# Kernel tuning notes

Hardware: AMD Instinct MI355X
Metric: run time of the kernel (lower is better)

The kernel has to match this reference:

```python
import jax, jax.numpy as jnp
import numpy as np

NUM_HEADS = 16
KEY_DIM = 64
NUM_FEATURES = 256
D_MODEL = NUM_HEADS * KEY_DIM
EPS = 1e-6


def softmax_kernel(data, proj):
    # data: [..., N, D], proj: [D, F]
    # Faithful to source: ratio uses proj.shape[0] (=D), matching the TF code.
    data_normalizer = 1.0 / jnp.sqrt(jnp.sqrt(jnp.asarray(data.shape[-1], data.dtype)))
    ratio = 1.0 / jnp.sqrt(jnp.asarray(proj.shape[0], data.dtype))
    data = data_normalizer * data
    data_dash = jnp.einsum('...nd,df->...nf', data, proj)
    diag = jnp.sum(jnp.square(data), axis=-1, keepdims=True)  # [..., N, 1]
    return ratio * (jnp.exp(data_dash - diag / 2.0) + EPS)


def setup_inputs() -> dict:
    key = jax.random.key(0)
    ks = jax.random.split(key, 12)
    B, N = 4, 4096
    s = 1.0 / np.sqrt(D_MODEL)
    inp = {
        'queries': jax.random.normal(ks[0], (B, N, D_MODEL), jnp.float32),
        'keys': jax.random.normal(ks[1], (B, N, D_MODEL), jnp.float32),
        'Wq': jax.random.normal(ks[2], (D_MODEL, D_MODEL), jnp.float32) * s,
        'bq': jnp.zeros((D_MODEL,), jnp.float32),
        'Wk': jax.random.normal(ks[3], (D_MODEL, D_MODEL), jnp.float32) * s,
        'bk': jnp.zeros((D_MODEL,), jnp.float32),
        'Wv': jax.random.normal(ks[4], (D_MODEL, D_MODEL), jnp.float32) * s,
        'bv': jnp.zeros((D_MODEL,), jnp.float32),
        'Wo': jax.random.normal(ks[5], (D_MODEL, D_MODEL), jnp.float32) * s,
        'bo': jnp.zeros((D_MODEL,), jnp.float32),
        # GlorotNormal for [KEY_DIM, NUM_FEATURES]
        'proj': jax.random.normal(ks[6], (KEY_DIM, NUM_FEATURES), jnp.float32)
                * np.sqrt(2.0 / (KEY_DIM + NUM_FEATURES)),
    }
    return inp


def reference(queries, keys, Wq, bq, Wk, bk, Wv, bv, Wo, bo, proj):
    # Original code uses x = queries for q, k, v (self-attention); keys arg unused.
    x = queries
    B, N, _ = x.shape
    H, D = NUM_HEADS, KEY_DIM

    def split_heads(t):
        return t.reshape(B, N, H, D).transpose(0, 2, 1, 3)  # [B,H,N,D]

    q = split_heads(x @ Wq + bq)
    k = split_heads(x @ Wk + bk)
    v = split_heads(x @ Wv + bv)

    q_prime = softmax_kernel(q, proj)  # [B,H,N,F]
    k_prime = softmax_kernel(k, proj)  # [B,H,N,F]

    kv = jnp.einsum('bhnf,bhnd->bhfd', k_prime, v)        # [B,H,F,D]
    qkv = jnp.einsum('bhnf,bhfd->bhnd', q_prime, kv)       # [B,H,N,D]
    k_sum = jnp.sum(k_prime, axis=2)                        # [B,H,F]
    norm = jnp.einsum('bhnf,bhf->bhn', q_prime, k_sum) + EPS
    qkv = qkv / norm[..., None]

    out = qkv.transpose(0, 2, 1, 3).reshape(B, N, H * D)    # [B,N,d_model]
    return out @ Wo + bo
```

## Files before the change

kernel.cpp:

```cpp
#include <hip/hip_runtime.h>

typedef __attribute__((ext_vector_type(8))) short short8;
typedef __attribute__((ext_vector_type(4))) float f32x4;

#define MFMA16 __builtin_amdgcn_mfma_f32_16x16x32_bf16

#define GLOAD16(gp, lp) __builtin_amdgcn_global_load_lds(                      \
    (const __attribute__((address_space(1))) void*)(gp),                       \
    (__attribute__((address_space(3))) void*)(lp), 16, 0, 0)

__device__ __forceinline__ unsigned short f2bf(float f) {
  unsigned int u = __float_as_uint(f);
  unsigned int r = u + 0x7fffu + ((u >> 16) & 1u);
  return (unsigned short)(r >> 16);
}
__device__ __forceinline__ float bf2f(unsigned short h) {
  return __uint_as_float(((unsigned int)h) << 16);
}

__global__ __launch_bounds__(256) void cast_x_kernel(
    const float* __restrict__ in, unsigned short* __restrict__ out, int n4) {
  int i = blockIdx.x * 256 + threadIdx.x;
  if (i >= n4) return;
  float4 v = reinterpret_cast<const float4*>(in)[i];
  ushort4 o;
  o.x = f2bf(v.x); o.y = f2bf(v.y); o.z = f2bf(v.z); o.w = f2bf(v.w);
  reinterpret_cast<ushort4*>(out)[i] = o;
}

__global__ __launch_bounds__(256) void tcast_f32_kernel(
    const float* __restrict__ in, unsigned short* __restrict__ out, int R, int C) {
  __shared__ float t[64][65];
  int c0 = blockIdx.x * 64, r0 = blockIdx.y * 64;
  int tx = threadIdx.x, ty = threadIdx.y;
#pragma unroll
  for (int i = 0; i < 16; ++i)
    t[ty + 4 * i][tx] = in[(size_t)(r0 + ty + 4 * i) * C + c0 + tx];
  __syncthreads();
#pragma unroll
  for (int i = 0; i < 16; ++i)
    out[(size_t)(c0 + ty + 4 * i) * R + r0 + tx] = f2bf(t[tx][ty + 4 * i]);
}

__global__ __launch_bounds__(256) void tcast4_kernel(
    const float* __restrict__ i0, const float* __restrict__ i1,
    const float* __restrict__ i2, const float* __restrict__ i3,
    unsigned short* __restrict__ o0, unsigned short* __restrict__ o1,
    unsigned short* __restrict__ o2, unsigned short* __restrict__ o3) {
  const float* in = i0; unsigned short* out = o0;
  if (blockIdx.z == 1) { in = i1; out = o1; }
  else if (blockIdx.z == 2) { in = i2; out = o2; }
  else if (blockIdx.z == 3) { in = i3; out = o3; }
  __shared__ float t[64][65];
  int c0 = blockIdx.x * 64, r0 = blockIdx.y * 64;
  int tx = threadIdx.x, ty = threadIdx.y;
#pragma unroll
  for (int i = 0; i < 16; ++i)
    t[ty + 4 * i][tx] = in[(size_t)(r0 + ty + 4 * i) * 1024 + c0 + tx];
  __syncthreads();
#pragma unroll
  for (int i = 0; i < 16; ++i)
    out[(size_t)(c0 + ty + 4 * i) * 1024 + r0 + tx] = f2bf(t[tx][ty + 4 * i]);
}

template <int OUTF>
__global__ __launch_bounds__(256) void gemm_bt_kernel(
    const unsigned short* __restrict__ A,
    const unsigned short* W0, const unsigned short* W1, const unsigned short* W2,
    const float* b0, const float* b1, const float* b2,
    void* o0, void* o1, void* o2) {
  constexpr int KD = 1024, ND = 1024;
  const unsigned short* W = W0; const float* bias = b0; void* op = o0;
  if (blockIdx.z == 1) { W = W1; bias = b1; op = o1; }
  else if (blockIdx.z == 2) { W = W2; bias = b2; op = o2; }

  __shared__ unsigned short lsA[128 * 32];
  __shared__ unsigned short lsB[128 * 32];
  extern __shared__ unsigned short tt[];
  int tid = threadIdx.x;
  int w = tid >> 6, lane = tid & 63;
  int m0 = blockIdx.x * 128, n0 = blockIdx.y * 128;
  int wm = (w >> 1) * 64, wn = (w & 1) * 64;

  int srow0 = (w * 2 + 0) * 16 + (lane >> 2);
  int srow1 = (w * 2 + 1) * 16 + (lane >> 2);
  int scol = (lane & 3) * 8;
  const unsigned short* gA0 = A + (size_t)(m0 + srow0) * KD + scol;
  const unsigned short* gA1 = A + (size_t)(m0 + srow1) * KD + scol;
  const unsigned short* gB0 = W + (size_t)(n0 + srow0) * KD + scol;
  const unsigned short* gB1 = W + (size_t)(n0 + srow1) * KD + scol;
  unsigned short* lA0 = &lsA[(w * 2 + 0) * 512];
  unsigned short* lA1 = &lsA[(w * 2 + 1) * 512];
  unsigned short* lB0 = &lsB[(w * 2 + 0) * 512];
  unsigned short* lB1 = &lsB[(w * 2 + 1) * 512];

  f32x4 acc[4][4];
#pragma unroll
  for (int fm = 0; fm < 4; ++fm)
#pragma unroll
    for (int fn = 0; fn < 4; ++fn) acc[fm][fn] = (f32x4){0.f, 0.f, 0.f, 0.f};

  for (int kt = 0; kt < KD; kt += 32) {
    GLOAD16(gA0 + kt, lA0);
    GLOAD16(gA1 + kt, lA1);
    GLOAD16(gB0 + kt, lB0);
    GLOAD16(gB1 + kt, lB1);
    __syncthreads();
    short8 af[4], bfr[4];
#pragma unroll
    for (int fm = 0; fm < 4; ++fm)
      af[fm] = *reinterpret_cast<const short8*>(
          &lsA[(wm + fm * 16 + (lane & 15)) * 32 + (lane >> 4) * 8]);
#pragma unroll
    for (int fn = 0; fn < 4; ++fn)
      bfr[fn] = *reinterpret_cast<const short8*>(
          &lsB[(wn + fn * 16 + (lane & 15)) * 32 + (lane >> 4) * 8]);
#pragma unroll
    for (int fm = 0; fm < 4; ++fm)
#pragma unroll
      for (int fn = 0; fn < 4; ++fn)
        acc[fm][fn] = MFMA16(af[fm], bfr[fn], acc[fm][fn], 0, 0, 0);
    __syncthreads();
  }

#pragma unroll
  for (int fn = 0; fn < 4; ++fn) {
    int coll = wn + fn * 16 + (lane & 15);
    float bv = bias[n0 + coll];
#pragma unroll
    for (int fm = 0; fm < 4; ++fm) {
#pragma unroll
      for (int j = 0; j < 4; ++j) {
        int rowl = wm + fm * 16 + (lane >> 4) * 4 + j;
        float v = acc[fm][fn][j] + bv;
        if constexpr (OUTF == 2) {
          tt[coll * 136 + rowl] = f2bf(v);
        } else if constexpr (OUTF == 1) {
          reinterpret_cast<float*>(op)[(size_t)(m0 + rowl) * ND + n0 + coll] = v;
        } else {
          reinterpret_cast<unsigned short*>(op)[(size_t)(m0 + rowl) * ND + n0 + coll] =
              f2bf(v);
        }
      }
    }
  }
  if constexpr (OUTF == 2) {
    __syncthreads();
    int b = m0 >> 12, tok0 = m0 & 4095;
    int c = tid >> 1, half = (tid & 1) * 64;
    unsigned short* dst = reinterpret_cast<unsigned short*>(op) +
                          (size_t)(b * 1024 + n0 + c) * 4096 + tok0 + half;
#pragma unroll
    for (int i = 0; i < 8; ++i) {
      short8 vv = *reinterpret_cast<const short8*>(&tt[c * 136 + half + i * 8]);
      *reinterpret_cast<short8*>(dst + i * 8) = vv;
    }
  }
}

__global__ __launch_bounds__(256) void kv_fused_kernel(
    const unsigned short* __restrict__ K, const unsigned short* __restrict__ PT,
    const unsigned short* __restrict__ VT,
    float* __restrict__ kvp0, float* __restrict__ kvp1, float* __restrict__ ksp) {
  __shared__ unsigned short kp[256 * 40];
  int s = blockIdx.x, bh = blockIdx.y, b = bh >> 4, h = bh & 15;
  int tid = threadIdx.x, w = tid >> 6, lane = tid & 63;
  int lo = lane & 15, hi = lane >> 4;
  int f0w = w * 64;
  float* kvp = (s < 8) ? kvp0 : kvp1;
  int sl = s & 7;

  short8 pb[4][2];
#pragma unroll
  for (int fn = 0; fn < 4; ++fn) {
    int f = f0w + fn * 16 + lo;
    pb[fn][0] = *reinterpret_cast<const short8*>(PT + (size_t)f * 64 + hi * 8);
    pb[fn][1] = *reinterpret_cast<const short8*>(PT + (size_t)f * 64 + 32 + hi * 8);
  }
  const unsigned short* vbase[4];
#pragma unroll
  for (int fn = 0; fn < 4; ++fn)
    vbase[fn] = VT + (size_t)(bh * 64 + fn * 16 + lo) * 4096;

  f32x4 acck[4][4];
#pragma unroll
  for (int fm = 0; fm < 4; ++fm)
#pragma unroll
    for (int fn = 0; fn < 4; ++fn) acck[fm][fn] = (f32x4){0.f, 0.f, 0.f, 0.f};
  float ks[4] = {0.f, 0.f, 0.f, 0.f};

  for (int c = 0; c < 8; ++c) {
    int n0 = s * 256 + c * 32;
    const unsigned short* Ab = K + (size_t)(b * 4096 + n0) * 1024 + h * 64;
    short8 af[2][2];
    float dp[2] = {0.f, 0.f};
#pragma unroll
    for (int fm = 0; fm < 2; ++fm)
#pragma unroll
      for (int kt = 0; kt < 2; ++kt) {
        af[fm][kt] = *reinterpret_cast<const short8*>(
            Ab + (size_t)(fm * 16 + lo) * 1024 + kt * 32 + hi * 8);
#pragma unroll
        for (int j = 0; j < 8; ++j) {
          float qv = bf2f((unsigned short)af[fm][kt][j]);
          dp[fm] += qv * qv;
        }
      }
#pragma unroll
    for (int fm = 0; fm < 2; ++fm) {
      dp[fm] += __shfl_xor(dp[fm], 16);
      dp[fm] += __shfl_xor(dp[fm], 32);
    }
    f32x4 accf[2][4];
#pragma unroll
    for (int fm = 0; fm < 2; ++fm)
#pragma unroll
      for (int fn = 0; fn < 4; ++fn) accf[fm][fn] = (f32x4){0.f, 0.f, 0.f, 0.f};
#pragma unroll
    for (int fn = 0; fn < 4; ++fn) {
      accf[0][fn] = MFMA16(af[0][0], pb[fn][0], accf[0][fn], 0, 0, 0);
      accf[0][fn] = MFMA16(af[0][1], pb[fn][1], accf[0][fn], 0, 0, 0);
      accf[1][fn] = MFMA16(af[1][0], pb[fn][0], accf[1][fn], 0, 0, 0);
      accf[1][fn] = MFMA16(af[1][1], pb[fn][1], accf[1][fn], 0, 0, 0);
    }
#pragma unroll
    for (int fm = 0; fm < 2; ++fm)
#pragma unroll
      for (int fn = 0; fn < 4; ++fn)
#pragma unroll
        for (int j = 0; j < 4; ++j) {
          float dg = __shfl(dp[fm], hi * 4 + j);
          float v = 0.125f *
                    (__expf(0.35355339059327373f * accf[fm][fn][j] - 0.0625f * dg) + 1e-6f);
          ks[fn] += v;
          kp[(f0w + fn * 16 + lo) * 40 + fm * 16 + hi * 4 + j] = f2bf(v);
        }
    short8 a2[4], b2[4];
#pragma unroll
    for (int fm = 0; fm < 4; ++fm)
      a2[fm] = *reinterpret_cast<const short8*>(&kp[(f0w + fm * 16 + lo) * 40 + hi * 8]);
#pragma unroll
    for (int fn = 0; fn < 4; ++fn)
      b2[fn] = *reinterpret_cast<const short8*>(vbase[fn] + n0 + hi * 8);
#pragma unroll
    for (int fm = 0; fm < 4; ++fm)
#pragma unroll
      for (int fn = 0; fn < 4; ++fn)
        acck[fm][fn] = MFMA16(a2[fm], b2[fn], acck[fm][fn], 0, 0, 0);
  }
#pragma unroll
  for (int fn = 0; fn < 4; ++fn) {
    float v = ks[fn];
    v += __shfl_xor(v, 16);
    v += __shfl_xor(v, 32);
    if (hi == 0)
      ksp[(size_t)(s * 64 + bh) * 256 + f0w + fn * 16 + lo] = v;
  }
#pragma unroll
  for (int fm = 0; fm < 4; ++fm)
#pragma unroll
    for (int fn = 0; fn < 4; ++fn)
#pragma unroll
      for (int j = 0; j < 4; ++j)
        kvp[((size_t)(sl * 64 + bh) * 256 + f0w + fm * 16 + hi * 4 + j) * 64 + fn * 16 + lo] =
            acck[fm][fn][j];
}

__global__ __launch_bounds__(256) void kvred_kernel(
    const float* __restrict__ kvp0, const float* __restrict__ kvp1,
    const float* __restrict__ ksp,
    unsigned short* __restrict__ kvT, float* __restrict__ ksum) {
  __shared__ float t[64][65];
  int bh = blockIdx.x, g = blockIdx.y, tid = threadIdx.x;
  int fbase = g * 64;
  int fo = tid >> 2, dq = (tid & 3) * 16;
  float sum[16];
#pragma unroll
  for (int i = 0; i < 16; ++i) sum[i] = 0.f;
#pragma unroll
  for (int s = 0; s < 16; ++s) {
    const float* base = ((s < 8) ? kvp0 : kvp1) +
                        ((size_t)((s & 7) * 64 + bh) * 256 + fbase + fo) * 64 + dq;
#pragma unroll
    for (int i = 0; i < 16; ++i) sum[i] += base[i];
  }
#pragma unroll
  for (int i = 0; i < 16; ++i) t[fo][dq + i] = sum[i];
  __syncthreads();
  int d = tid >> 2, fq = (tid & 3) * 16;
  unsigned short wv[16];
#pragma unroll
  for (int i = 0; i < 16; ++i) wv[i] = f2bf(t[fq + i][d]);
  unsigned short* dst = kvT + (size_t)(bh * 64 + d) * 256 + fbase + fq;
  *reinterpret_cast<short8*>(dst) = *reinterpret_cast<const short8*>(&wv[0]);
  *reinterpret_cast<short8*>(dst + 8) = *reinterpret_cast<const short8*>(&wv[8]);
  if (g == 0) {
    float tsum = 0.f;
#pragma unroll
    for (int s = 0; s < 16; ++s) tsum += ksp[(size_t)(s * 64 + bh) * 256 + tid];
    ksum[bh * 256 + tid] = tsum;
  }
}

__global__ __launch_bounds__(256) void qkv_fused_kernel(
    const unsigned short* __restrict__ Q, const unsigned short* __restrict__ PT,
    const unsigned short* __restrict__ KVT, const float* __restrict__ KSUM,
    unsigned short* __restrict__ Y) {
  __shared__ unsigned short qp[128 * 128];
  int bh = blockIdx.y, b = bh >> 4, h = bh & 15;
  int t0 = blockIdx.x * 128;
  int tid = threadIdx.x, w = tid >> 6, lane = tid & 63;
  int lo = lane & 15, hi = lane >> 4;
  int r0 = w * 32;
  const unsigned short* Ab = Q + (size_t)(b * 4096 + t0 + r0) * 1024 + h * 64;

  float ksr[16];
#pragma unroll
  for (int fn = 0; fn < 16; ++fn) ksr[fn] = KSUM[bh * 256 + fn * 16 + lo];

  short8 af[2][2];
  float dp[2] = {0.f, 0.f};
#pragma unroll
  for (int fm = 0; fm < 2; ++fm)
#pragma unroll
    for (int kt = 0; kt < 2; ++kt) {
      af[fm][kt] = *reinterpret_cast<const short8*>(
          Ab + (size_t)(fm * 16 + lo) * 1024 + kt * 32 + hi * 8);
#pragma unroll
      for (int j = 0; j < 8; ++j) {
        float qv = bf2f((unsigned short)af[fm][kt][j]);
        dp[fm] += qv * qv;
      }
    }
#pragma unroll
  for (int fm = 0; fm < 2; ++fm) {
    dp[fm] += __shfl_xor(dp[fm], 16);
    dp[fm] += __shfl_xor(dp[fm], 32);
  }

  float np[2][4] = {{0.f, 0.f, 0.f, 0.f}, {0.f, 0.f, 0.f, 0.f}};
  f32x4 acco[2][4];
#pragma unroll
  for (int fm = 0; fm < 2; ++fm)
#pragma unroll
    for (int fn = 0; fn < 4; ++fn) acco[fm][fn] = (f32x4){0.f, 0.f, 0.f, 0.f};

#pragma unroll
  for (int hf = 0; hf < 2; ++hf) {
    f32x4 accf[2][8];
#pragma unroll
    for (int fm = 0; fm < 2; ++fm)
#pragma unroll
      for (int fn = 0; fn < 8; ++fn) accf[fm][fn] = (f32x4){0.f, 0.f, 0.f, 0.f};
#pragma unroll
    for (int fn = 0; fn < 8; ++fn) {
      int f = hf * 128 + fn * 16 + lo;
      short8 pb0 = *reinterpret_cast<const short8*>(PT + (size_t)f * 64 + hi * 8);
      short8 pb1 = *reinterpret_cast<const short8*>(PT + (size_t)f * 64 + 32 + hi * 8);
      accf[0][fn] = MFMA16(af[0][0], pb0, accf[0][fn], 0, 0, 0);
      accf[0][fn] = MFMA16(af[0][1], pb1, accf[0][fn], 0, 0, 0);
      accf[1][fn] = MFMA16(af[1][0], pb0, accf[1][fn], 0, 0, 0);
      accf[1][fn] = MFMA16(af[1][1], pb1, accf[1][fn], 0, 0, 0);
    }
#pragma unroll
    for (int fm = 0; fm < 2; ++fm)
#pragma unroll
      for (int fn = 0; fn < 8; ++fn)
#pragma unroll
        for (int j = 0; j < 4; ++j) {
          float dg = __shfl(dp[fm], hi * 4 + j);
          float v = 0.125f *
                    (__expf(0.35355339059327373f * accf[fm][fn][j] - 0.0625f * dg) + 1e-6f);
          np[fm][j] += v * ksr[hf * 8 + fn];
          int row = r0 + fm * 16 + hi * 4 + j;
          int fl = fn * 16 + lo;
          int byt = (row * 256 + fl * 2) ^ ((row & 7) << 4);
          *reinterpret_cast<unsigned short*>(reinterpret_cast<char*>(qp) + byt) = f2bf(v);
        }
#pragma unroll
    for (int kt2 = 0; kt2 < 4; ++kt2) {
      short8 a2[2], b2[4];
#pragma unroll
      for (int fm = 0; fm < 2; ++fm) {
        int row = r0 + fm * 16 + lo;
        int byt = (row * 256 + kt2 * 64 + hi * 16) ^ ((row & 7) << 4);
        a2[fm] = *reinterpret_cast<const short8*>(reinterpret_cast<char*>(qp) + byt);
      }
#pragma unroll
      for (int fn = 0; fn < 4; ++fn)
        b2[fn] = *reinterpret_cast<const short8*>(
            KVT + (size_t)(bh * 64 + fn * 16 + lo) * 256 + hf * 128 + kt2 * 32 + hi * 8);
#pragma unroll
      for (int fm = 0; fm < 2; ++fm)
#pragma unroll
        for (int fn = 0; fn < 4; ++fn)
          acco[fm][fn] = MFMA16(a2[fm], b2[fn], acco[fm][fn], 0, 0, 0);
    }
  }
#pragma unroll
  for (int fm = 0; fm < 2; ++fm)
#pragma unroll
    for (int j = 0; j < 4; ++j) {
      np[fm][j] += __shfl_xor(np[fm][j], 1);
      np[fm][j] += __shfl_xor(np[fm][j], 2);
      np[fm][j] += __shfl_xor(np[fm][j], 4);
      np[fm][j] += __shfl_xor(np[fm][j], 8);
    }
#pragma unroll
  for (int fm = 0; fm < 2; ++fm)
#pragma unroll
    for (int j = 0; j < 4; ++j) {
      float nv = np[fm][j] + 1e-6f;
      int row = b * 4096 + t0 + r0 + fm * 16 + hi * 4 + j;
#pragma unroll
      for (int fn = 0; fn < 4; ++fn)
        Y[(size_t)row * 1024 + h * 64 + fn * 16 + lo] = f2bf(acco[fm][fn][j] / nv);
    }
}

extern "C" void kernel_launch(void* const* d_in, const int* in_sizes, int n_in,
                              void* d_out, int out_size, void* d_ws, size_t ws_size,
                              hipStream_t stream) {
  (void)in_sizes; (void)n_in; (void)out_size; (void)ws_size;
  const float* x    = (const float*)d_in[0];
  const float* Wq   = (const float*)d_in[2];
  const float* bq   = (const float*)d_in[3];
  const float* Wk   = (const float*)d_in[4];
  const float* bk   = (const float*)d_in[5];
  const float* Wv   = (const float*)d_in[6];
  const float* bv   = (const float*)d_in[7];
  const float* Wo   = (const float*)d_in[8];
  const float* bo   = (const float*)d_in[9];
  const float* proj = (const float*)d_in[10];
  float* out = (float*)d_out;

  constexpr size_t SZ_XB = (size_t)16384 * 1024 * 2;
  constexpr size_t SZ_W  = (size_t)1024 * 1024 * 2;
  constexpr size_t SZ_PT = (size_t)256 * 64 * 2;

  char* p = (char*)d_ws;
  size_t off = 0;
  char* a_xb  = p + off; off += SZ_XB;
  char* a_WqT = p + off; off += SZ_W;
  char* a_WkT = p + off; off += SZ_W;
  char* a_WvT = p + off; off += SZ_W;
  char* a_WoT = p + off; off += SZ_W;
  char* a_pT  = p + off; off += SZ_PT;
  char* a_qb  = p + off; off += SZ_XB;
  char* a_kb  = p + off; off += SZ_XB;
  char* a_ksp  = p + off; off += (size_t)16 * 64 * 256 * 4;
  char* a_kvT  = p + off; off += (size_t)64 * 64 * 256 * 2;
  char* a_ksum = p + off; off += (size_t)64 * 256 * 4;

  char* a_kvp0 = a_xb;
  char* a_kvp1 = (char*)d_out + SZ_XB;
  char* a_vT = (char*)d_out;
  char* a_y = a_kb;

  dim3 tb(64, 4);

  cast_x_kernel<<<16384, 256, 0, stream>>>(x, (unsigned short*)a_xb, 16384 * 1024 / 4);
  tcast4_kernel<<<dim3(16, 16, 4), tb, 0, stream>>>(
      Wq, Wk, Wv, Wo,
      (unsigned short*)a_WqT, (unsigned short*)a_WkT,
      (unsigned short*)a_WvT, (unsigned short*)a_WoT);
  tcast_f32_kernel<<<dim3(4, 1), tb, 0, stream>>>(proj, (unsigned short*)a_pT, 64, 256);

  gemm_bt_kernel<0><<<dim3(128, 8, 2), 256, 0, stream>>>(
      (unsigned short*)a_xb,
      (unsigned short*)a_WqT, (unsigned short*)a_WkT, nullptr,
      bq, bk, nullptr, a_qb, a_kb, nullptr);
  gemm_bt_kernel<2><<<dim3(128, 8, 1), 256, 128 * 136 * 2, stream>>>(
      (unsigned short*)a_xb,
      (unsigned short*)a_WvT, nullptr, nullptr,
      bv, nullptr, nullptr, a_vT, nullptr, nullptr);

  kv_fused_kernel<<<dim3(16, 64), 256, 0, stream>>>(
      (unsigned short*)a_kb, (unsigned short*)a_pT, (unsigned short*)a_vT,
      (float*)a_kvp0, (float*)a_kvp1, (float*)a_ksp);
  kvred_kernel<<<dim3(64, 4), 256, 0, stream>>>(
      (float*)a_kvp0, (float*)a_kvp1, (float*)a_ksp,
      (unsigned short*)a_kvT, (float*)a_ksum);

  qkv_fused_kernel<<<dim3(32, 64), 256, 0, stream>>>(
      (unsigned short*)a_qb, (unsigned short*)a_pT, (unsigned short*)a_kvT,
      (float*)a_ksum, (unsigned short*)a_y);

  gemm_bt_kernel<1><<<dim3(128, 8, 1), 256, 0, stream>>>(
      (unsigned short*)a_y,
      (unsigned short*)a_WoT, nullptr, nullptr,
      bo, nullptr, nullptr, out, nullptr, nullptr);
}
```

Baseline: 373.6 us.

## Merge Q/K/V projection GEMMs into one launch and halve KV split count

The separate Q/K and V projection GEMM launches become a single three-way batched launch, with the V slice writing transposed output through shared memory. The kv_fused kernel now processes 512 tokens per block over 8 splits instead of 16, which halves the partial KV buffers and the work in the reduction kernel. The V loads are moved earlier to overlap with the exp computation, and the K-prime shared-memory stores are packed into ushort4 writes. Fewer splits mean fewer blocks (512) for kv_fused, which may reduce occupancy, and all GEMM blocks now reserve dynamic shared memory.

```diff
diff --git a/kernel.cpp b/kernel.cpp
--- a/kernel.cpp
+++ b/kernel.cpp
@@ -123,6 +123,7 @@
     __syncthreads();
   }
 
+  bool vpath = (OUTF == 3) && (blockIdx.z == 2);
 #pragma unroll
   for (int fn = 0; fn < 4; ++fn) {
     int coll = wn + fn * 16 + (lane & 15);
@@ -133,27 +134,30 @@
       for (int j = 0; j < 4; ++j) {
         int rowl = wm + fm * 16 + (lane >> 4) * 4 + j;
         float v = acc[fm][fn][j] + bv;
-        if constexpr (OUTF == 2) {
-          tt[coll * 136 + rowl] = f2bf(v);
-        } else if constexpr (OUTF == 1) {
+        if constexpr (OUTF == 1) {
           reinterpret_cast<float*>(op)[(size_t)(m0 + rowl) * ND + n0 + coll] = v;
         } else {
-          reinterpret_cast<unsigned short*>(op)[(size_t)(m0 + rowl) * ND + n0 + coll] =
-              f2bf(v);
+          if (vpath)
+            tt[coll * 136 + rowl] = f2bf(v);
+          else
+            reinterpret_cast<unsigned short*>(op)[(size_t)(m0 + rowl) * ND + n0 + coll] =
+                f2bf(v);
         }
       }
     }
   }
-  if constexpr (OUTF == 2) {
-    __syncthreads();
-    int b = m0 >> 12, tok0 = m0 & 4095;
-    int c = tid >> 1, half = (tid & 1) * 64;
-    unsigned short* dst = reinterpret_cast<unsigned short*>(op) +
-                          (size_t)(b * 1024 + n0 + c) * 4096 + tok0 + half;
-#pragma unroll
-    for (int i = 0; i < 8; ++i) {
-      short8 vv = *reinterpret_cast<const short8*>(&tt[c * 136 + half + i * 8]);
-      *reinterpret_cast<short8*>(dst + i * 8) = vv;
+  if constexpr (OUTF == 3) {
+    if (vpath) {
+      __syncthreads();
+      int b = m0 >> 12, tok0 = m0 & 4095;
+      int c = tid >> 1, half = (tid & 1) * 64;
+      unsigned short* dst = reinterpret_cast<unsigned short*>(op) +
+                            (size_t)(b * 1024 + n0 + c) * 4096 + tok0 + half;
+#pragma unroll
+      for (int i = 0; i < 8; ++i) {
+        short8 vv = *reinterpret_cast<const short8*>(&tt[c * 136 + half + i * 8]);
+        *reinterpret_cast<short8*>(dst + i * 8) = vv;
+      }
     }
   }
 }
@@ -161,14 +165,12 @@
 __global__ __launch_bounds__(256) void kv_fused_kernel(
     const unsigned short* __restrict__ K, const unsigned short* __restrict__ PT,
     const unsigned short* __restrict__ VT,
-    float* __restrict__ kvp0, float* __restrict__ kvp1, float* __restrict__ ksp) {
+    float* __restrict__ kvp, float* __restrict__ ksp) {
   __shared__ unsigned short kp[256 * 40];
   int s = blockIdx.x, bh = blockIdx.y, b = bh >> 4, h = bh & 15;
   int tid = threadIdx.x, w = tid >> 6, lane = tid & 63;
   int lo = lane & 15, hi = lane >> 4;
   int f0w = w * 64;
-  float* kvp = (s < 8) ? kvp0 : kvp1;
-  int sl = s & 7;
 
   short8 pb[4][2];
 #pragma unroll
@@ -189,23 +191,30 @@
     for (int fn = 0; fn < 4; ++fn) acck[fm][fn] = (f32x4){0.f, 0.f, 0.f, 0.f};
   float ks[4] = {0.f, 0.f, 0.f, 0.f};
 
-  for (int c = 0; c < 8; ++c) {
-    int n0 = s * 256 + c * 32;
+  for (int c = 0; c < 16; ++c) {
+    int n0 = s * 512 + c * 32;
     const unsigned short* Ab = K + (size_t)(b * 4096 + n0) * 1024 + h * 64;
-    short8 af[2][2];
-    float dp[2] = {0.f, 0.f};
-#pragma unroll
-    for (int fm = 0; fm < 2; ++fm)
-#pragma unroll
-      for (int kt = 0; kt < 2; ++kt) {
+    short8 af[2][2], b2[4];
+#pragma unroll
+    for (int fm = 0; fm < 2; ++fm)
+#pragma unroll
+      for (int kt = 0; kt < 2; ++kt)
         af[fm][kt] = *reinterpret_cast<const short8*>(
             Ab + (size_t)(fm * 16 + lo) * 1024 + kt * 32 + hi * 8);
+#pragma unroll
+    for (int fn = 0; fn < 4; ++fn)
+      b2[fn] = *reinterpret_cast<const short8*>(vbase[fn] + n0 + hi * 8);
+
+    float dp[2] = {0.f, 0.f};
+#pragma unroll
+    for (int fm = 0; fm < 2; ++fm)
+#pragma unroll
+      for (int kt = 0; kt < 2; ++kt)
 #pragma unroll
         for (int j = 0; j < 8; ++j) {
           float qv = bf2f((unsigned short)af[fm][kt][j]);
           dp[fm] += qv * qv;
         }
-      }
 #pragma unroll
     for (int fm = 0; fm < 2; ++fm) {
       dp[fm] += __shfl_xor(dp[fm], 16);
@@ -226,22 +235,22 @@
 #pragma unroll
     for (int fm = 0; fm < 2; ++fm)
 #pragma unroll
-      for (int fn = 0; fn < 4; ++fn)
+      for (int fn = 0; fn < 4; ++fn) {
+        ushort4 pk;
 #pragma unroll
         for (int j = 0; j < 4; ++j) {
           float dg = __shfl(dp[fm], hi * 4 + j);
           float v = 0.125f *
                     (__expf(0.35355339059327373f * accf[fm][fn][j] - 0.0625f * dg) + 1e-6f);
           ks[fn] += v;
-          kp[(f0w + fn * 16 + lo) * 40 + fm * 16 + hi * 4 + j] = f2bf(v);
+          ((unsigned short*)&pk)[j] = f2bf(v);
         }
-    short8 a2[4], b2[4];
+        *reinterpret_cast<ushort4*>(&kp[(f0w + fn * 16 + lo) * 40 + fm * 16 + hi * 4]) = pk;
+      }
+    short8 a2[4];
 #pragma unroll
     for (int fm = 0; fm < 4; ++fm)
       a2[fm] = *reinterpret_cast<const short8*>(&kp[(f0w + fm * 16 + lo) * 40 + hi * 8]);
-#pragma unroll
-    for (int fn = 0; fn < 4; ++fn)
-      b2[fn] = *reinterpret_cast<const short8*>(vbase[fn] + n0 + hi * 8);
 #pragma unroll
     for (int fm = 0; fm < 4; ++fm)
 #pragma unroll
@@ -262,13 +271,12 @@
     for (int fn = 0; fn < 4; ++fn)
 #pragma unroll
       for (int j = 0; j < 4; ++j)
-        kvp[((size_t)(sl * 64 + bh) * 256 + f0w + fm * 16 + hi * 4 + j) * 64 + fn * 16 + lo] =
+        kvp[((size_t)(s * 64 + bh) * 256 + f0w + fm * 16 + hi * 4 + j) * 64 + fn * 16 + lo] =
             acck[fm][fn][j];
 }
 
 __global__ __launch_bounds__(256) void kvred_kernel(
-    const float* __restrict__ kvp0, const float* __restrict__ kvp1,
-    const float* __restrict__ ksp,
+    const float* __restrict__ kvp, const float* __restrict__ ksp,
     unsigned short* __restrict__ kvT, float* __restrict__ ksum) {
   __shared__ float t[64][65];
   int bh = blockIdx.x, g = blockIdx.y, tid = threadIdx.x;
@@ -278,9 +286,8 @@
 #pragma unroll
   for (int i = 0; i < 16; ++i) sum[i] = 0.f;
 #pragma unroll
-  for (int s = 0; s < 16; ++s) {
-    const float* base = ((s < 8) ? kvp0 : kvp1) +
-                        ((size_t)((s & 7) * 64 + bh) * 256 + fbase + fo) * 64 + dq;
+  for (int s = 0; s < 8; ++s) {
+    const float* base = kvp + ((size_t)(s * 64 + bh) * 256 + fbase + fo) * 64 + dq;
 #pragma unroll
     for (int i = 0; i < 16; ++i) sum[i] += base[i];
   }
@@ -297,7 +304,7 @@
   if (g == 0) {
     float tsum = 0.f;
 #pragma unroll
-    for (int s = 0; s < 16; ++s) tsum += ksp[(size_t)(s * 64 + bh) * 256 + tid];
+    for (int s = 0; s < 8; ++s) tsum += ksp[(size_t)(s * 64 + bh) * 256 + tid];
     ksum[bh * 256 + tid] = tsum;
   }
 }
@@ -448,12 +455,11 @@
   char* a_pT  = p + off; off += SZ_PT;
   char* a_qb  = p + off; off += SZ_XB;
   char* a_kb  = p + off; off += SZ_XB;
-  char* a_ksp  = p + off; off += (size_t)16 * 64 * 256 * 4;
+  char* a_ksp  = p + off; off += (size_t)8 * 64 * 256 * 4;
   char* a_kvT  = p + off; off += (size_t)64 * 64 * 256 * 2;
   char* a_ksum = p + off; off += (size_t)64 * 256 * 4;
 
-  char* a_kvp0 = a_xb;
-  char* a_kvp1 = (char*)d_out + SZ_XB;
+  char* a_kvp = a_xb;
   char* a_vT = (char*)d_out;
   char* a_y = a_kb;
 
@@ -466,21 +472,16 @@
       (unsigned short*)a_WvT, (unsigned short*)a_WoT);
   tcast_f32_kernel<<<dim3(4, 1), tb, 0, stream>>>(proj, (unsigned short*)a_pT, 64, 256);
 
-  gemm_bt_kernel<0><<<dim3(128, 8, 2), 256, 0, stream>>>(
+  gemm_bt_kernel<3><<<dim3(128, 8, 3), 256, 128 * 136 * 2, stream>>>(
       (unsigned short*)a_xb,
-      (unsigned short*)a_WqT, (unsigned short*)a_WkT, nullptr,
-      bq, bk, nullptr, a_qb, a_kb, nullptr);
-  gemm_bt_kernel<2><<<dim3(128, 8, 1), 256, 128 * 136 * 2, stream>>>(
-      (unsigned short*)a_xb,
-      (unsigned short*)a_WvT, nullptr, nullptr,
-      bv, nullptr, nullptr, a_vT, nullptr, nullptr);
-
-  kv_fused_kernel<<<dim3(16, 64), 256, 0, stream>>>(
+      (unsigned short*)a_WqT, (unsigned short*)a_WkT, (unsigned short*)a_WvT,
+      bq, bk, bv, a_qb, a_kb, a_vT);
+
+  kv_fused_kernel<<<dim3(8, 64), 256, 0, stream>>>(
       (unsigned short*)a_kb, (unsigned short*)a_pT, (unsigned short*)a_vT,
-      (float*)a_kvp0, (float*)a_kvp1, (float*)a_ksp);
+      (float*)a_kvp, (float*)a_ksp);
   kvred_kernel<<<dim3(64, 4), 256, 0, stream>>>(
-      (float*)a_kvp0, (float*)a_kvp1, (float*)a_ksp,
-      (unsigned short*)a_kvT, (float*)a_ksum);
+      (float*)a_kvp, (float*)a_ksp, (unsigned short*)a_kvT, (float*)a_ksum);
 
   qkv_fused_kernel<<<dim3(32, 64), 256, 0, stream>>>(
       (unsigned short*)a_qb, (unsigned short*)a_pT, (unsigned short*)a_kvT,
```

Result: faster. 342.3 us (-8.4%).
